# Optimization experiments

Measured on AMD Instinct MI355X. Metric: run time of the kernel, lower is better.

## Reference

```python
import jax, jax.numpy as jnp
from jax import lax
import numpy as np

# Mamba mixer dims (mamba-1.4b scale)
D_MODEL, D_INNER, D_STATE, D_CONV, DT_RANK = 2048, 4096, 16, 4, 128
B, L = 2, 1024


def setup_inputs() -> dict:
    key = jax.random.key(0)
    ks = jax.random.split(key, 10)
    s = 0.02
    x = jax.random.normal(ks[0], (B, L, D_MODEL), jnp.float32)
    W_in = jax.random.normal(ks[1], (2 * D_INNER, D_MODEL), jnp.float32) * s
    conv_w = jax.random.normal(ks[2], (D_INNER, D_CONV), jnp.float32) * s  # depthwise kernel
    conv_b = jax.random.normal(ks[3], (D_INNER,), jnp.float32) * s
    W_x = jax.random.normal(ks[4], (DT_RANK + 2 * D_STATE, D_INNER), jnp.float32) * s
    W_dt = jax.random.normal(ks[5], (D_INNER, DT_RANK), jnp.float32) * s
    b_dt = jax.random.normal(ks[6], (D_INNER,), jnp.float32) * s
    # S4D-real init: A = -[1..d_state] per channel
    A_log = jnp.log(jnp.broadcast_to(jnp.arange(1, D_STATE + 1, dtype=jnp.float32), (D_INNER, D_STATE)))
    Dp = jnp.ones((D_INNER,), jnp.float32)
    W_out = jax.random.normal(ks[7], (D_MODEL, D_INNER), jnp.float32) * s
    return {"x": x, "W_in": W_in, "conv_w": conv_w, "conv_b": conv_b,
            "W_x": W_x, "W_dt": W_dt, "b_dt": b_dt, "A_log": A_log,
            "Dp": Dp, "W_out": W_out}


def reference(x, W_in, conv_w, conv_b, W_x, W_dt, b_dt, A_log, Dp, W_out):
    b, l, _ = x.shape
    d_inner, d_state = A_log.shape
    dt_rank = W_dt.shape[1]
    d_conv = conv_w.shape[1]

    # in_proj -> x branch and gate z   [b,l,2*d_inner]
    xz = jnp.einsum('bld,ed->ble', x, W_in)
    xp, z = jnp.split(xz, 2, axis=-1)

    # causal depthwise conv1d (kernel size d_conv) + SiLU
    xpad = jnp.pad(xp, ((0, 0), (d_conv - 1, 0), (0, 0)))
    xc = conv_b + sum(xpad[:, k:k + l, :] * conv_w[:, k] for k in range(d_conv))
    xc = jax.nn.silu(xc)

    # input-dependent dt, B, C
    dbc = jnp.einsum('ble,fe->blf', xc, W_x)
    dt = dbc[..., :dt_rank]
    Bm = dbc[..., dt_rank:dt_rank + d_state]          # [b,l,s]
    Cm = dbc[..., dt_rank + d_state:]                 # [b,l,s]
    delta = jax.nn.softplus(jnp.einsum('blr,er->ble', dt, W_dt) + b_dt)  # [b,l,e]

    A = -jnp.exp(A_log)                               # [e,s]
    dA = jnp.exp(delta[..., None] * A)                # [b,l,e,s]
    dBx = delta[..., None] * Bm[:, :, None, :] * xc[..., None]  # [b,l,e,s]

    def step(h, inp):
        dA_t, dBx_t = inp                             # [b,e,s]
        h = dA_t * h + dBx_t
        return h, h

    h0 = jnp.zeros((b, d_inner, d_state), x.dtype)
    _, hs = lax.scan(step, h0, (jnp.swapaxes(dA, 0, 1), jnp.swapaxes(dBx, 0, 1)))
    hs = jnp.swapaxes(hs, 0, 1)                       # [b,l,e,s]

    y = jnp.einsum('bles,bls->ble', hs, Cm) + xc * Dp
    y = y * jax.nn.silu(z)
    return jnp.einsum('ble,de->bld', y, W_out)
```

## Files before the change

### kernel.cpp

```cpp
#include <hip/hip_runtime.h>
#include <cstdint>


typedef __bf16 bf16x8 __attribute__((ext_vector_type(8)));
typedef float f32x4 __attribute__((ext_vector_type(4)));

__device__ __forceinline__ unsigned short f2bf(float f) {
  uint32_t u = __float_as_uint(f);
  u += 0x7FFFu + ((u >> 16) & 1u);
  return (unsigned short)(u >> 16);
}

__device__ __forceinline__ float silu_f(float v) {
  return v / (1.f + __expf(-v));
}

__device__ __forceinline__ float softplus_f(float v) {
  return (v > 20.f) ? v : log1pf(__expf(v));
}

__global__ void cast_f32_to_bf16(const float* __restrict__ src,
                                 unsigned short* __restrict__ dst, int n4) {
  int i = blockIdx.x * 256 + threadIdx.x;
  if (i >= n4) return;
  float4 v = reinterpret_cast<const float4*>(src)[i];
  ushort4 o;
  o.x = f2bf(v.x); o.y = f2bf(v.y); o.z = f2bf(v.z); o.w = f2bf(v.w);
  reinterpret_cast<ushort4*>(dst)[i] = o;
}

__global__ void cast_wx_pad(const float* __restrict__ Wx,
                            unsigned short* __restrict__ dst) {
  int i = blockIdx.x * 256 + threadIdx.x;
  int r = i >> 12;
  float v = (r < 160) ? Wx[(size_t)r * 4096 + (i & 4095)] : 0.f;
  dst[i] = f2bf(v);
}

#define BM 128
#define BN 128
#define BKK 32

__device__ __forceinline__ void stage_tile(const unsigned short* __restrict__ G,
                                           int ldK, int g0, int k0,
                                           unsigned short* lds, int wave, int lane) {
#pragma unroll
  for (int c = 0; c < 2; ++c) {
    int row = c * 64 + wave * 16 + (lane >> 2);
    int col = (lane & 3) * 8;
    const unsigned short* src = G + (size_t)(g0 + row) * ldK + (k0 + col);
    unsigned short* dst = lds + c * 2048 + wave * 512;
    __builtin_amdgcn_global_load_lds((__attribute__((address_space(1))) void*)(src),
                                     (__attribute__((address_space(3))) void*)(dst),
                                     16, 0, 0);
  }
}

__global__ __launch_bounds__(256)
void gemm_bt(const unsigned short* __restrict__ A, const unsigned short* __restrict__ B,
             float* __restrict__ C, int M, int N, int ldK, int kchunk,
             const float* __restrict__ bias_sp) {
  __shared__ unsigned short As[BM * BKK];
  __shared__ unsigned short Bs[BN * BKK];
  const int tid = threadIdx.x;
  const int wave = tid >> 6, lane = tid & 63;
  const int wr = wave >> 1, wc = wave & 1;
  const int m0 = blockIdx.y * BM, n0 = blockIdx.x * BN;
  const int lr = lane & 15, lg = lane >> 4;
  const int kb = blockIdx.z * kchunk, ke = kb + kchunk;
  C += (size_t)blockIdx.z * M * N;

  f32x4 zero = {0.f, 0.f, 0.f, 0.f};
  f32x4 acc[4][4];
#pragma unroll
  for (int i = 0; i < 4; ++i)
#pragma unroll
    for (int j = 0; j < 4; ++j) acc[i][j] = zero;

  for (int k0 = kb; k0 < ke; k0 += BKK) {
    stage_tile(A, ldK, m0, k0, As, wave, lane);
    stage_tile(B, ldK, n0, k0, Bs, wave, lane);
    __syncthreads();
    bf16x8 af[4], bfr[4];
#pragma unroll
    for (int i = 0; i < 4; ++i)
      af[i] = *reinterpret_cast<const bf16x8*>(&As[(wr * 64 + i * 16 + lr) * BKK + lg * 8]);
#pragma unroll
    for (int j = 0; j < 4; ++j)
      bfr[j] = *reinterpret_cast<const bf16x8*>(&Bs[(wc * 64 + j * 16 + lr) * BKK + lg * 8]);
#pragma unroll
    for (int i = 0; i < 4; ++i)
#pragma unroll
      for (int j = 0; j < 4; ++j)
        acc[i][j] = __builtin_amdgcn_mfma_f32_16x16x32_bf16(af[i], bfr[j], acc[i][j], 0, 0, 0);
    __syncthreads();
  }

#pragma unroll
  for (int i = 0; i < 4; ++i) {
#pragma unroll
    for (int j = 0; j < 4; ++j) {
      int mrow = m0 + wr * 64 + i * 16 + lg * 4;
      int ncol = n0 + wc * 64 + j * 16 + lr;
      if (bias_sp) {
        float bv = bias_sp[ncol];
#pragma unroll
        for (int r = 0; r < 4; ++r)
          C[(size_t)(mrow + r) * N + ncol] = softplus_f(acc[i][j][r] + bv);
      } else {
#pragma unroll
        for (int r = 0; r < 4; ++r)
          C[(size_t)(mrow + r) * N + ncol] = acc[i][j][r];
      }
    }
  }
}

__global__ void reduce8_dbc(const float* __restrict__ p, float* __restrict__ dbc,
                            unsigned short* __restrict__ dt_bf) {
  int i = blockIdx.x * 256 + threadIdx.x;
  float s = 0.f;
#pragma unroll
  for (int c = 0; c < 8; ++c) s += p[(size_t)c * 524288 + i];
  dbc[i] = s;
  int col = i & 255;
  if (col < 128) dt_bf[(size_t)(i >> 8) * 128 + col] = f2bf(s);
}

__global__ void reduce2_out(const float* __restrict__ p, float* __restrict__ out) {
  int i = blockIdx.x * 256 + threadIdx.x;
  const float4* p4 = reinterpret_cast<const float4*>(p);
  float4 a = p4[i], b = p4[i + 1048576];
  float4 r; r.x = a.x + b.x; r.y = a.y + b.y; r.z = a.z + b.z; r.w = a.w + b.w;
  reinterpret_cast<float4*>(out)[i] = r;
}

__global__ __launch_bounds__(512, 2)
void gemm_bt_8ph(const unsigned short* __restrict__ A,
                 const unsigned short* __restrict__ B,
                 float* __restrict__ C, int M, int N, int K, int nbm) {
  __shared__ unsigned short As[2][8192];
  __shared__ unsigned short Bs[2][8192];
  const int tid = threadIdx.x;
  const int wid = tid >> 6, lane = tid & 63;
  const int wr = wid >> 2, wc = wid & 3;
  const int lr = lane & 15, lg = lane >> 4;

  const int cpx = gridDim.x >> 3;
  const int x = blockIdx.x;
  const int wg = (x & 7) * cpx + (x >> 3);
  const int bm = wg % nbm, bn = wg / nbm;
  const int m0 = bm * 256, n0 = bn * 256;

  const int srow = lane >> 2;
  const int scol = ((lane & 3) * 8) ^ (((lane >> 3) & 3) << 3);
  const unsigned short* Abase = A + (size_t)(m0 + wid * 32 + srow) * K + scol;
  const unsigned short* Bbase = B + (size_t)(n0 + wid * 32 + srow) * K + scol;

  const int swz = ((lr >> 1) & 3) << 3;
  const int aoff = (((wr * 128 + lr) * 32) + lg * 8) ^ swz;
  const int boff = (((wc * 64 + lr) * 32) + lg * 8) ^ swz;

  f32x4 acc[8][4];
  f32x4 zero = {0.f, 0.f, 0.f, 0.f};
#pragma unroll
  for (int i = 0; i < 8; ++i)
#pragma unroll
    for (int j = 0; j < 4; ++j) acc[i][j] = zero;

  const int nt = K / 32;

  auto STAGE = [&](int t) {
    const int buf = t & 1;
    const unsigned short* ap = Abase + t * 32;
    const unsigned short* bp = Bbase + t * 32;
#pragma unroll
    for (int c = 0; c < 2; ++c) {
      __builtin_amdgcn_global_load_lds(
          (__attribute__((address_space(1))) const void*)(ap + (size_t)c * 16 * K),
          (__attribute__((address_space(3))) void*)(&As[buf][wid * 1024 + c * 512]),
          16, 0, 0);
      __builtin_amdgcn_global_load_lds(
          (__attribute__((address_space(1))) const void*)(bp + (size_t)c * 16 * K),
          (__attribute__((address_space(3))) void*)(&Bs[buf][wid * 1024 + c * 512]),
          16, 0, 0);
    }
  };

  auto PHASE = [&](int buf) {
    bf16x8 a[8], b[4];
#pragma unroll
    for (int mf = 0; mf < 8; ++mf)
      a[mf] = *reinterpret_cast<const bf16x8*>(&As[buf][aoff + mf * 512]);
#pragma unroll
    for (int nf = 0; nf < 4; ++nf)
      b[nf] = *reinterpret_cast<const bf16x8*>(&Bs[buf][boff + nf * 512]);
    asm volatile("s_waitcnt lgkmcnt(0)" ::: "memory");
    __builtin_amdgcn_sched_barrier(0);
    __builtin_amdgcn_s_setprio(1);
#pragma unroll
    for (int nf = 0; nf < 4; ++nf)
#pragma unroll
      for (int mf = 0; mf < 8; ++mf)
        acc[mf][nf] = __builtin_amdgcn_mfma_f32_16x16x32_bf16(a[mf], b[nf], acc[mf][nf], 0, 0, 0);
    __builtin_amdgcn_s_setprio(0);
  };

  STAGE(0);
  STAGE(1);
  for (int t = 0; t < nt; t += 2) {
    asm volatile("s_waitcnt vmcnt(4)" ::: "memory");
    __builtin_amdgcn_s_barrier();
    PHASE(0);
    __builtin_amdgcn_s_barrier();
    if (t + 2 < nt) {
      STAGE(t + 2);
      asm volatile("s_waitcnt vmcnt(4)" ::: "memory");
    } else {
      asm volatile("s_waitcnt vmcnt(0)" ::: "memory");
    }
    __builtin_amdgcn_s_barrier();
    PHASE(1);
    __builtin_amdgcn_s_barrier();
    if (t + 3 < nt) STAGE(t + 3);
  }

#pragma unroll
  for (int mf = 0; mf < 8; ++mf) {
#pragma unroll
    for (int nf = 0; nf < 4; ++nf) {
      int mrow = m0 + wr * 128 + mf * 16 + lg * 4;
      int ncol = n0 + wc * 64 + nf * 16 + lr;
#pragma unroll
      for (int r = 0; r < 4; ++r)
        C[(size_t)(mrow + r) * N + ncol] = acc[mf][nf][r];
    }
  }
}

__global__ void conv_silu_kernel(const float* __restrict__ xz,
                                 const float* __restrict__ conv_w,
                                 const float* __restrict__ conv_b,
                                 float* __restrict__ xc,
                                 unsigned short* __restrict__ xc_bf) {
  int idx = blockIdx.x * 256 + threadIdx.x;
  int e = idx & 4095;
  int m = idx >> 12;
  int l = m & 1023;
  float acc = conv_b[e];
#pragma unroll
  for (int k = 0; k < 4; ++k) {
    int ls = l - 3 + k;
    if (ls >= 0) acc = fmaf(xz[(size_t)(m - 3 + k) * 8192 + e], conv_w[e * 4 + k], acc);
  }
  float s = silu_f(acc);
  xc[idx] = s;
  xc_bf[idx] = f2bf(s);
}

__global__ __launch_bounds__(256)
void scan_pass1(const float* __restrict__ delta, const float* __restrict__ dbc,
                const float* __restrict__ xc, const float* __restrict__ A_log,
                float* __restrict__ hfin, float* __restrict__ Pprod) {
  __shared__ float Bsh[1024];
  const int tid = threadIdx.x;
  const int bc = blockIdx.x >> 4;
  const int eg = blockIdx.x & 15;
  const int b = bc >> 4, c = bc & 15;
  const int e = eg * 256 + tid;
  const int mb = b * 1024 + c * 64;
  for (int i = tid; i < 1024; i += 256)
    Bsh[i] = dbc[(size_t)(mb + (i >> 4)) * 256 + 128 + (i & 15)];
  __syncthreads();

  float A[16];
  const float4* al = reinterpret_cast<const float4*>(A_log + (size_t)e * 16);
#pragma unroll
  for (int q = 0; q < 4; ++q) {
    float4 v = al[q];
    A[q * 4 + 0] = -__expf(v.x); A[q * 4 + 1] = -__expf(v.y);
    A[q * 4 + 2] = -__expf(v.z); A[q * 4 + 3] = -__expf(v.w);
  }
  float h[16], P[16];
#pragma unroll
  for (int s = 0; s < 16; ++s) { h[s] = 0.f; P[s] = 1.f; }

  for (int ll = 0; ll < 64; ++ll) {
    const size_t m = (size_t)(mb + ll);
    float dl = delta[m * 4096 + e];
    float dxc = dl * xc[m * 4096 + e];
#pragma unroll
    for (int s = 0; s < 16; ++s) {
      float dA = __expf(dl * A[s]);
      P[s] *= dA;
      h[s] = fmaf(dA, h[s], Bsh[ll * 16 + s] * dxc);
    }
  }
  float* hp = hfin + ((size_t)bc * 4096 + e) * 16;
  float* pp = Pprod + ((size_t)bc * 4096 + e) * 16;
#pragma unroll
  for (int s = 0; s < 16; ++s) { hp[s] = h[s]; pp[s] = P[s]; }
}

__global__ void scan_pass2(float* __restrict__ hfin, const float* __restrict__ Pprod) {
  int idx = blockIdx.x * 256 + threadIdx.x;
  int b = idx >> 16;
  int es = idx & 65535;
  float H = 0.f;
  for (int c = 0; c < 16; ++c) {
    size_t o = ((size_t)(b * 16 + c) << 16) + es;
    float hf = hfin[o];
    float Pp = Pprod[o];
    hfin[o] = H;
    H = fmaf(Pp, H, hf);
  }
}

__global__ __launch_bounds__(256)
void scan_pass3(const float* __restrict__ delta, const float* __restrict__ dbc,
                const float* __restrict__ xc, const float* __restrict__ xz,
                const float* __restrict__ A_log, const float* __restrict__ Dp,
                const float* __restrict__ hcarry, unsigned short* __restrict__ y_bf) {
  __shared__ float Bsh[1024];
  __shared__ float Csh[1024];
  const int tid = threadIdx.x;
  const int bc = blockIdx.x >> 4;
  const int eg = blockIdx.x & 15;
  const int b = bc >> 4, c = bc & 15;
  const int e = eg * 256 + tid;
  const int mb = b * 1024 + c * 64;
  for (int i = tid; i < 1024; i += 256) {
    size_t base = (size_t)(mb + (i >> 4)) * 256 + (i & 15);
    Bsh[i] = dbc[base + 128];
    Csh[i] = dbc[base + 144];
  }
  __syncthreads();

  float A[16];
  const float4* al = reinterpret_cast<const float4*>(A_log + (size_t)e * 16);
#pragma unroll
  for (int q = 0; q < 4; ++q) {
    float4 v = al[q];
    A[q * 4 + 0] = -__expf(v.x); A[q * 4 + 1] = -__expf(v.y);
    A[q * 4 + 2] = -__expf(v.z); A[q * 4 + 3] = -__expf(v.w);
  }
  float h[16];
  const float* hp = hcarry + ((size_t)bc * 4096 + e) * 16;
#pragma unroll
  for (int s = 0; s < 16; ++s) h[s] = hp[s];
  const float Dv = Dp[e];

  for (int ll = 0; ll < 64; ++ll) {
    const size_t m = (size_t)(mb + ll);
    float dl = delta[m * 4096 + e];
    float xcv = xc[m * 4096 + e];
    float dxc = dl * xcv;
    float y = 0.f;
#pragma unroll
    for (int s = 0; s < 16; ++s) {
      float dA = __expf(dl * A[s]);
      h[s] = fmaf(dA, h[s], Bsh[ll * 16 + s] * dxc);
      y = fmaf(h[s], Csh[ll * 16 + s], y);
    }
    float z = xz[m * 8192 + 4096 + e];
    y = (y + xcv * Dv) * silu_f(z);
    y_bf[m * 4096 + e] = f2bf(y);
  }
}

extern "C" void kernel_launch(void* const* d_in, const int* in_sizes, int n_in,
                              void* d_out, int out_size, void* d_ws, size_t ws_size,
                              hipStream_t stream) {
  const float* x      = (const float*)d_in[0];
  const float* W_in   = (const float*)d_in[1];
  const float* conv_w = (const float*)d_in[2];
  const float* conv_b = (const float*)d_in[3];
  const float* W_x    = (const float*)d_in[4];
  const float* W_dt   = (const float*)d_in[5];
  const float* b_dt   = (const float*)d_in[6];
  const float* A_log  = (const float*)d_in[7];
  const float* Dp     = (const float*)d_in[8];
  const float* W_out  = (const float*)d_in[9];
  float* out = (float*)d_out;
  char* ws = (char*)d_ws;

  unsigned short* Win_bf    = (unsigned short*)(ws + 0);
  float*          gpart     = (float*)(ws + 0);
  float*          delta     = (float*)(ws + 0);
  unsigned short* x_bf      = (unsigned short*)(ws + 33554432);
  unsigned short* y_bf      = (unsigned short*)(ws + 33554432);
  unsigned short* Wout_bf   = (unsigned short*)(ws + 50331648);
  unsigned short* Wx_bf     = (unsigned short*)(ws + 67108864);
  unsigned short* Wdt_bf    = (unsigned short*)(ws + 69206016);
  float*          xz        = (float*)(ws + 70254592);
  float*          xc        = (float*)(ws + 137363456);
  unsigned short* xc_bf     = (unsigned short*)(ws + 170917888);
  float*          hfin      = (float*)(ws + 170917888);
  float*          Pprod     = (float*)(ws + 179306496);
  float*          dbc       = (float*)(ws + 187695104);
  unsigned short* dt_bf     = (unsigned short*)(ws + 189792256);

  cast_f32_to_bf16<<<4096, 256, 0, stream>>>(x, x_bf, 1048576);
  cast_f32_to_bf16<<<16384, 256, 0, stream>>>(W_in, Win_bf, 4194304);
  cast_f32_to_bf16<<<8192, 256, 0, stream>>>(W_out, Wout_bf, 2097152);
  cast_wx_pad<<<4096, 256, 0, stream>>>(W_x, Wx_bf);
  cast_f32_to_bf16<<<512, 256, 0, stream>>>(W_dt, Wdt_bf, 131072);

  gemm_bt_8ph<<<256, 512, 0, stream>>>(x_bf, Win_bf, xz, 2048, 8192, 2048, 8);

  conv_silu_kernel<<<32768, 256, 0, stream>>>(xz, conv_w, conv_b, xc, xc_bf);

  gemm_bt<<<dim3(2, 16, 8), 256, 0, stream>>>(xc_bf, Wx_bf, gpart, 2048, 256, 4096, 512, nullptr);
  reduce8_dbc<<<2048, 256, 0, stream>>>(gpart, dbc, dt_bf);

  gemm_bt<<<dim3(32, 16, 1), 256, 0, stream>>>(dt_bf, Wdt_bf, delta, 2048, 4096, 128, 128, b_dt);

  scan_pass1<<<512, 256, 0, stream>>>(delta, dbc, xc, A_log, hfin, Pprod);
  scan_pass2<<<512, 256, 0, stream>>>(hfin, Pprod);
  scan_pass3<<<512, 256, 0, stream>>>(delta, dbc, xc, xz, A_log, Dp, hfin, y_bf);

  gemm_bt<<<dim3(16, 16, 2), 256, 0, stream>>>(y_bf, Wout_bf, gpart, 2048, 2048, 4096, 2048, nullptr);
  reduce2_out<<<4096, 256, 0, stream>>>(gpart, out);
}
```

Baseline: 389.9 us.

## Restructure bf16 GEMM into K=64 tiles with quarter-staged prefetch and 4-phase MFMA

The GEMM now works on K=64 tiles, which doubles the LDS buffers to 128 KB total and uses a row-XOR swizzle for the new 64-wide rows. Global-to-LDS loads are split into four quarter loads (A top/bottom, B top/bottom). These are interleaved between four MFMA sub-phases, so prefetch of the next tile overlaps compute and the per-iteration barrier count drops. The larger LDS footprint may limit occupancy to one block per CU, despite launch_bounds(512,2). The tighter buffer-reuse ordering also risks LDS hazards.

```diff
diff --git a/kernel.cpp b/kernel.cpp
--- a/kernel.cpp
+++ b/kernel.cpp
@@ -139,8 +139,8 @@
 void gemm_bt_8ph(const unsigned short* __restrict__ A,
                  const unsigned short* __restrict__ B,
                  float* __restrict__ C, int M, int N, int K, int nbm) {
-  __shared__ unsigned short As[2][8192];
-  __shared__ unsigned short Bs[2][8192];
+  __shared__ unsigned short As[2][16384];
+  __shared__ unsigned short Bs[2][16384];
   const int tid = threadIdx.x;
   const int wid = tid >> 6, lane = tid & 63;
   const int wr = wid >> 2, wc = wid & 3;
@@ -152,14 +152,8 @@
   const int bm = wg % nbm, bn = wg / nbm;
   const int m0 = bm * 256, n0 = bn * 256;
 
-  const int srow = lane >> 2;
-  const int scol = ((lane & 3) * 8) ^ (((lane >> 3) & 3) << 3);
-  const unsigned short* Abase = A + (size_t)(m0 + wid * 32 + srow) * K + scol;
-  const unsigned short* Bbase = B + (size_t)(n0 + wid * 32 + srow) * K + scol;
-
-  const int swz = ((lr >> 1) & 3) << 3;
-  const int aoff = (((wr * 128 + lr) * 32) + lg * 8) ^ swz;
-  const int boff = (((wc * 64 + lr) * 32) + lg * 8) ^ swz;
+  const int strow = tid >> 3;
+  const int stcol0 = (tid & 7) * 8;
 
   f32x4 acc[8][4];
   f32x4 zero = {0.f, 0.f, 0.f, 0.f};
@@ -168,61 +162,113 @@
 #pragma unroll
     for (int j = 0; j < 4; ++j) acc[i][j] = zero;
 
-  const int nt = K / 32;
-
-  auto STAGE = [&](int t) {
+  const int nt = K / 64;
+
+  auto QUANT = [&](int t, int q) {
     const int buf = t & 1;
-    const unsigned short* ap = Abase + t * 32;
-    const unsigned short* bp = Bbase + t * 32;
-#pragma unroll
-    for (int c = 0; c < 2; ++c) {
+    const unsigned short* G = (q < 2) ? A : B;
+    const int g0 = ((q < 2) ? m0 : n0) + ((q & 1) ? 128 : 0);
+    unsigned short* lds = ((q < 2) ? &As[buf][0] : &Bs[buf][0]) + ((q & 1) ? 8192 : 0);
+    const int k0 = t * 64;
+#pragma unroll
+    for (int r = 0; r < 2; ++r) {
+      int row = r * 64 + strow;
+      int scol = stcol0 ^ ((row & 7) << 3);
+      const unsigned short* src = G + (size_t)(g0 + row) * K + (k0 + scol);
       __builtin_amdgcn_global_load_lds(
-          (__attribute__((address_space(1))) const void*)(ap + (size_t)c * 16 * K),
-          (__attribute__((address_space(3))) void*)(&As[buf][wid * 1024 + c * 512]),
+          (__attribute__((address_space(1))) const void*)(src),
+          (__attribute__((address_space(3))) void*)(lds + r * 4096 + tid * 8),
           16, 0, 0);
-      __builtin_amdgcn_global_load_lds(
-          (__attribute__((address_space(1))) const void*)(bp + (size_t)c * 16 * K),
-          (__attribute__((address_space(3))) void*)(&Bs[buf][wid * 1024 + c * 512]),
-          16, 0, 0);
     }
   };
 
-  auto PHASE = [&](int buf) {
-    bf16x8 a[8], b[4];
-#pragma unroll
-    for (int mf = 0; mf < 8; ++mf)
-      a[mf] = *reinterpret_cast<const bf16x8*>(&As[buf][aoff + mf * 512]);
-#pragma unroll
-    for (int nf = 0; nf < 4; ++nf)
-      b[nf] = *reinterpret_cast<const bf16x8*>(&Bs[buf][boff + nf * 512]);
+  auto RD_A = [&](int buf, int mf, int ks) -> bf16x8 {
+    int row = wr * 128 + mf * 16 + lr;
+    int col = (ks * 32 + lg * 8) ^ ((row & 7) << 3);
+    return *reinterpret_cast<const bf16x8*>(&As[buf][row * 64 + col]);
+  };
+  auto RD_B = [&](int buf, int nf, int ks) -> bf16x8 {
+    int row = wc * 64 + nf * 16 + lr;
+    int col = (ks * 32 + lg * 8) ^ ((row & 7) << 3);
+    return *reinterpret_cast<const bf16x8*>(&Bs[buf][row * 64 + col]);
+  };
+
+  QUANT(0, 0); QUANT(0, 1); QUANT(0, 2); QUANT(0, 3);
+  QUANT(1, 0);
+
+  bf16x8 a[4][2], b[4][2];
+  for (int t = 0; t < nt; ++t) {
+    const int buf = t & 1;
+    const bool pf1 = (t + 1 < nt);
+    if (pf1) {
+      QUANT(t + 1, 1);
+      asm volatile("s_waitcnt vmcnt(4)" ::: "memory");
+    } else {
+      asm volatile("s_waitcnt vmcnt(0)" ::: "memory");
+    }
+    __builtin_amdgcn_s_barrier();
+#pragma unroll
+    for (int mf = 0; mf < 4; ++mf)
+#pragma unroll
+      for (int ks = 0; ks < 2; ++ks) a[mf][ks] = RD_A(buf, mf, ks);
+#pragma unroll
+    for (int nf = 0; nf < 2; ++nf)
+#pragma unroll
+      for (int ks = 0; ks < 2; ++ks) b[nf][ks] = RD_B(buf, nf, ks);
     asm volatile("s_waitcnt lgkmcnt(0)" ::: "memory");
     __builtin_amdgcn_sched_barrier(0);
     __builtin_amdgcn_s_setprio(1);
 #pragma unroll
-    for (int nf = 0; nf < 4; ++nf)
-#pragma unroll
-      for (int mf = 0; mf < 8; ++mf)
-        acc[mf][nf] = __builtin_amdgcn_mfma_f32_16x16x32_bf16(a[mf], b[nf], acc[mf][nf], 0, 0, 0);
+    for (int nf = 0; nf < 2; ++nf)
+#pragma unroll
+      for (int mf = 0; mf < 4; ++mf)
+#pragma unroll
+        for (int ks = 0; ks < 2; ++ks)
+          acc[mf][nf] = __builtin_amdgcn_mfma_f32_16x16x32_bf16(a[mf][ks], b[nf][ks], acc[mf][nf], 0, 0, 0);
     __builtin_amdgcn_s_setprio(0);
-  };
-
-  STAGE(0);
-  STAGE(1);
-  for (int t = 0; t < nt; t += 2) {
-    asm volatile("s_waitcnt vmcnt(4)" ::: "memory");
+    if (pf1) QUANT(t + 1, 2);
+#pragma unroll
+    for (int nf = 2; nf < 4; ++nf)
+#pragma unroll
+      for (int ks = 0; ks < 2; ++ks) b[nf][ks] = RD_B(buf, nf, ks);
+    asm volatile("s_waitcnt lgkmcnt(0)" ::: "memory");
+    __builtin_amdgcn_sched_barrier(0);
+    __builtin_amdgcn_s_setprio(1);
+#pragma unroll
+    for (int nf = 2; nf < 4; ++nf)
+#pragma unroll
+      for (int mf = 0; mf < 4; ++mf)
+#pragma unroll
+        for (int ks = 0; ks < 2; ++ks)
+          acc[mf][nf] = __builtin_amdgcn_mfma_f32_16x16x32_bf16(a[mf][ks], b[nf][ks], acc[mf][nf], 0, 0, 0);
+    __builtin_amdgcn_s_setprio(0);
+    if (pf1) QUANT(t + 1, 3);
+#pragma unroll
+    for (int mf = 0; mf < 4; ++mf)
+#pragma unroll
+      for (int ks = 0; ks < 2; ++ks) a[mf][ks] = RD_A(buf, mf + 4, ks);
+    asm volatile("s_waitcnt lgkmcnt(0)" ::: "memory");
+    __builtin_amdgcn_sched_barrier(0);
+    __builtin_amdgcn_s_setprio(1);
+#pragma unroll
+    for (int nf = 0; nf < 2; ++nf)
+#pragma unroll
+      for (int mf = 0; mf < 4; ++mf)
+#pragma unroll
+        for (int ks = 0; ks < 2; ++ks)
+          acc[mf + 4][nf] = __builtin_amdgcn_mfma_f32_16x16x32_bf16(a[mf][ks], b[nf][ks], acc[mf + 4][nf], 0, 0, 0);
+    __builtin_amdgcn_s_setprio(0);
     __builtin_amdgcn_s_barrier();
-    PHASE(0);
-    __builtin_amdgcn_s_barrier();
-    if (t + 2 < nt) {
-      STAGE(t + 2);
-      asm volatile("s_waitcnt vmcnt(4)" ::: "memory");
-    } else {
-      asm volatile("s_waitcnt vmcnt(0)" ::: "memory");
-    }
-    __builtin_amdgcn_s_barrier();
-    PHASE(1);
-    __builtin_amdgcn_s_barrier();
-    if (t + 3 < nt) STAGE(t + 3);
+    if (t + 2 < nt) QUANT(t + 2, 0);
+    __builtin_amdgcn_s_setprio(1);
+#pragma unroll
+    for (int nf = 2; nf < 4; ++nf)
+#pragma unroll
+      for (int mf = 0; mf < 4; ++mf)
+#pragma unroll
+        for (int ks = 0; ks < 2; ++ks)
+          acc[mf + 4][nf] = __builtin_amdgcn_mfma_f32_16x16x32_bf16(a[mf][ks], b[nf][ks], acc[mf + 4][nf], 0, 0, 0);
+    __builtin_amdgcn_s_setprio(0);
   }
 
 #pragma unroll
```

New measurement: 384.7 us. No clear change (-1.3%).
